# Kernel tuning notes

Hardware: AMD Instinct MI355X
Metric: run time of the kernel (lower is better)

The kernel has to match this reference:

```python
import jax, jax.numpy as jnp
import numpy as np

DEPTH = 8
DIM = 512
D_INNER = 2 * DIM          # mamba expand=2
D_STATE = 16
D_CONV = 4
DT_RANK = DIM // 16        # 32
B, H, W = 2, 16, 16
EPS = 1e-5


def setup_inputs() -> dict:
    key = jax.random.key(0)
    ks = jax.random.split(key, 8)
    s = 0.02
    f32 = jnp.float32
    x = jax.random.normal(ks[0], (B, DIM, H, W), f32)
    in_proj_w = (jax.random.normal(ks[1], (DEPTH, 2 * D_INNER, DIM), f32) * s)
    conv_w = (jax.random.normal(ks[2], (DEPTH, D_INNER, D_CONV), f32) * 0.1)
    conv_b = jnp.zeros((DEPTH, D_INNER), f32)
    x_proj_w = (jax.random.normal(ks[3], (DEPTH, DT_RANK + 2 * D_STATE, D_INNER), f32) * s)
    dt_proj_w = (jax.random.normal(ks[4], (DEPTH, D_INNER, DT_RANK), f32) * s)
    dt_proj_b = (jax.random.normal(ks[5], (DEPTH, D_INNER), f32) * 0.1)
    # S4D-real init: A = -exp(A_log), A_log = log(1..d_state)
    A_log = jnp.log(jnp.broadcast_to(
        jnp.arange(1, D_STATE + 1, dtype=f32), (DEPTH, D_INNER, D_STATE)))
    D = jnp.ones((DEPTH, D_INNER), f32)
    out_proj_w = (jax.random.normal(ks[6], (DEPTH, DIM, D_INNER), f32) * s)
    norm_w = jnp.ones((DEPTH, DIM), f32)
    final_norm_w = jnp.ones((DIM,), f32)
    return {"x": x, "in_proj_w": in_proj_w, "conv_w": conv_w, "conv_b": conv_b,
            "x_proj_w": x_proj_w, "dt_proj_w": dt_proj_w, "dt_proj_b": dt_proj_b,
            "A_log": A_log, "D": D, "out_proj_w": out_proj_w,
            "norm_w": norm_w, "final_norm_w": final_norm_w}


def _rmsnorm(x, w):
    # rms_norm_ref: no mean subtraction, weight only (bias is None)
    return x * jax.lax.rsqrt(jnp.mean(x * x, axis=-1, keepdims=True) + EPS) * w


def _mixer(h, Wi, cw, cb, Wx, Wdt, bdt, A_log, Dv, Wo):
    # h: [B, L, DIM]
    xz = jnp.einsum('bld,ed->ble', h, Wi)            # [B,L,2*Di]
    xc, z = jnp.split(xz, 2, axis=-1)
    # causal depthwise conv1d (pad left d_conv-1), then SiLU
    xt = xc.transpose(0, 2, 1)                        # [B,Di,L]
    xt = jax.lax.conv_general_dilated(
        xt, cw[:, None, :], (1,), [(D_CONV - 1, 0)],
        feature_group_count=D_INNER)
    xc = jax.nn.silu((xt + cb[None, :, None]).transpose(0, 2, 1))  # [B,L,Di]
    dbl = jnp.einsum('bld,kd->blk', xc, Wx)           # [B,L,dt_rank+2N]
    dtr = dbl[..., :DT_RANK]
    Bm = dbl[..., DT_RANK:DT_RANK + D_STATE]          # [B,L,N]
    Cm = dbl[..., DT_RANK + D_STATE:]                 # [B,L,N]
    dt = jax.nn.softplus(jnp.einsum('blr,dr->bld', dtr, Wdt) + bdt)  # [B,L,Di]
    A = -jnp.exp(A_log)                               # [Di,N]
    dA = jnp.exp(dt[..., None] * A)                   # [B,L,Di,N]
    dBx = (dt * xc)[..., None] * Bm[:, :, None, :]    # [B,L,Di,N]

    def step(s, inp):
        a, bx, c = inp
        s = a * s + bx                                # [B,Di,N]
        return s, jnp.einsum('bdn,bn->bd', s, c)

    s0 = jnp.zeros((xc.shape[0], D_INNER, D_STATE), xc.dtype)
    _, ys = jax.lax.scan(step, s0, (dA.transpose(1, 0, 2, 3),
                                    dBx.transpose(1, 0, 2, 3),
                                    Cm.transpose(1, 0, 2)))
    y = ys.transpose(1, 0, 2) + Dv * xc               # [B,L,Di]
    y = y * jax.nn.silu(z)
    return jnp.einsum('bld,od->blo', y, Wo)           # [B,L,DIM]


def reference(x, in_proj_w, conv_w, conv_b, x_proj_w, dt_proj_w, dt_proj_b,
              A_log, D, out_proj_w, norm_w, final_norm_w):
    Bz, C, Hh, Ww = x.shape
    h = x.reshape(Bz, C, Hh * Ww).transpose(0, 2, 1)  # [B,L,C]
    residual = None
    for i in range(DEPTH):
        # fused add + RMSNorm (prenorm): residual <- h + residual; hn = norm(residual)
        residual = h if residual is None else h + residual
        hn = _rmsnorm(residual, norm_w[i])
        h = _mixer(hn, in_proj_w[i], conv_w[i], conv_b[i], x_proj_w[i],
                   dt_proj_w[i], dt_proj_b[i], A_log[i], D[i], out_proj_w[i])
    # Original module: with return_index=[depth-1], the returned tensor is the
    # post-loop `residual`; the final mixer output and final norm are dead code.
    out = residual.reshape(Bz, Hh, Ww, C)
    return out.transpose(0, 3, 1, 2)
```

## Files before the change

kernel.cpp:

```cpp
#include <hip/hip_runtime.h>
#include <hip/hip_bf16.h>

typedef __bf16 bf16x8 __attribute__((ext_vector_type(8)));
typedef __bf16 bf16x4 __attribute__((ext_vector_type(4)));
typedef float  f32x4  __attribute__((ext_vector_type(4)));

#define DIM    512
#define DINNER 1024
#define SEQL   256
#define NLAYER 7
#define LPAD   260
#define NCH    8
#define CLEN   32

#define N4WI (NLAYER * 2048 * 512 / 4)
#define N4WX (NLAYER * 64 * 1024 / 4)
#define N4WO (NLAYER * 512 * 1024 / 4)
#define N4ALL (N4WI + N4WX + N4WO)
#define NCASTB (N4ALL / 256)

__global__ __launch_bounds__(256) void k_castin(const float* __restrict__ Wi,
                                                const float* __restrict__ Wx,
                                                const float* __restrict__ Wo,
                                                const float* __restrict__ x,
                                                __hip_bfloat16* __restrict__ wib,
                                                __hip_bfloat16* __restrict__ wxb,
                                                __hip_bfloat16* __restrict__ wob,
                                                float* __restrict__ res,
                                                float* __restrict__ dblraw) {
  if (blockIdx.x >= NCASTB + 1024) {
    int i = (blockIdx.x - NCASTB - 1024) * 256 + threadIdx.x;
    reinterpret_cast<float4*>(dblraw)[i] = float4{0.f, 0.f, 0.f, 0.f};
    return;
  }
  if (blockIdx.x >= NCASTB) {
    int idx = (blockIdx.x - NCASTB) * 256 + threadIdx.x;
    int d = idx & (DIM - 1), l = (idx >> 9) & (SEQL - 1), b = idx >> 17;
    res[idx] = x[((size_t)((b << 9) + d) << 8) + l];
    return;
  }
  int i = blockIdx.x * 256 + threadIdx.x;
  const float* src; __hip_bfloat16* dst; int j;
  if (i < N4WI)             { src = Wi; dst = wib; j = i; }
  else if (i < N4WI + N4WX) { src = Wx; dst = wxb; j = i - N4WI; }
  else                      { src = Wo; dst = wob; j = i - N4WI - N4WX; }
  float4 v = reinterpret_cast<const float4*>(src)[j];
  struct alignas(8) B4 { __hip_bfloat16 a, b, c, d; };
  B4 o{ (__hip_bfloat16)v.x, (__hip_bfloat16)v.y, (__hip_bfloat16)v.z, (__hip_bfloat16)v.w };
  reinterpret_cast<B4*>(dst)[j] = o;
}

__global__ __launch_bounds__(1024) void k_front(const float* __restrict__ res,
                                                const float* __restrict__ nwL,
                                                const __hip_bfloat16* __restrict__ wiL,
                                                const __hip_bfloat16* __restrict__ wxL,
                                                const float4* __restrict__ cwL,
                                                const float* __restrict__ cbL,
                                                __hip_bfloat16* __restrict__ xcb,
                                                float* __restrict__ zT,
                                                float* __restrict__ dblraw) {
  __shared__ __align__(16) char smem[79872];
  __hip_bfloat16 (*s_hn)[520] = (__hip_bfloat16(*)[520])smem;
  float (*s_xz)[132] = (float(*)[132])(smem + 49920);
  __hip_bfloat16 (*s_xcb)[72] = (__hip_bfloat16(*)[72])(smem + 75264);
  const int tid = threadIdx.x, bid = blockIdx.x;
  const int wid = tid >> 6, lane = tid & 63;
  const int r = lane & 15, g = lane >> 4;
  const int ttile = bid >> 4, sl = bid & 15;
  const int t0 = ttile * 32, m0 = t0 - 3;
#pragma unroll
  for (int k = 0; k < 3; ++k) {
    int rw = wid * 3 + k;
    int grc = min(max(m0 + rw, 0), 511);
    const float* rr = res + ((size_t)grc << 9);
    float v[8]; float ssum = 0.f;
#pragma unroll
    for (int j2 = 0; j2 < 8; ++j2) { v[j2] = rr[lane + (j2 << 6)]; ssum = fmaf(v[j2], v[j2], ssum); }
#pragma unroll
    for (int m = 1; m < 64; m <<= 1) ssum += __shfl_xor(ssum, m);
    float inv = rsqrtf(ssum * (1.0f / 512.0f) + 1e-5f);
#pragma unroll
    for (int j2 = 0; j2 < 8; ++j2)
      s_hn[rw][lane + (j2 << 6)] = (__hip_bfloat16)(v[j2] * inv * nwL[lane + (j2 << 6)]);
  }
  __syncthreads();
  for (int j = wid; j < 24; j += 16) {
    int mf = j >> 3, cf = j & 7;
    int gcol = (cf < 4) ? (sl * 64 + cf * 16 + r) : (1024 + sl * 64 + (cf - 4) * 16 + r);
    const bf16x8* pb = reinterpret_cast<const bf16x8*>(wiL + (size_t)gcol * 512) + g;
    f32x4 acc = {0.f, 0.f, 0.f, 0.f};
#pragma unroll
    for (int kc = 0; kc < 16; ++kc) {
      bf16x8 a = *reinterpret_cast<const bf16x8*>(&s_hn[mf * 16 + r][kc * 32 + g * 8]);
      acc = __builtin_amdgcn_mfma_f32_16x16x32_bf16(a, pb[kc * 4], acc, 0, 0, 0);
    }
    int cc = (cf < 4) ? (cf * 16 + r) : (64 + (cf - 4) * 16 + r);
#pragma unroll
    for (int jj = 0; jj < 4; ++jj) s_xz[mf * 16 + g * 4 + jj][cc] = acc[jj];
  }
  __syncthreads();
  const int t0s = t0 & 255;
#pragma unroll
  for (int k = 0; k < 2; ++k) {
    int e = tid + (k << 10);
    int lloc = e >> 6, c = e & 63;
    int gd = sl * 64 + c;
    int lseq = t0s + lloc;
    float4 wv = cwL[gd];
    float accv = cbL[gd];
    accv = fmaf(s_xz[lloc + 3][c], wv.w, accv);
    if (lseq >= 1) accv = fmaf(s_xz[lloc + 2][c], wv.z, accv);
    if (lseq >= 2) accv = fmaf(s_xz[lloc + 1][c], wv.y, accv);
    if (lseq >= 3) accv = fmaf(s_xz[lloc + 0][c], wv.x, accv);
    float sv = accv / (1.f + __expf(-accv));
    __hip_bfloat16 hb = (__hip_bfloat16)sv;
    xcb[(size_t)(t0 + lloc) * 1024 + gd] = hb;
    s_xcb[lloc][c] = hb;
  }
  __syncthreads();
  if (wid < 8) {
    int mf = wid & 1, nf = wid >> 1;
    f32x4 acc = {0.f, 0.f, 0.f, 0.f};
#pragma unroll
    for (int kc = 0; kc < 2; ++kc) {
      bf16x8 a = *reinterpret_cast<const bf16x8*>(&s_xcb[mf * 16 + r][kc * 32 + g * 8]);
      bf16x8 bb = *reinterpret_cast<const bf16x8*>(
          wxL + (size_t)(nf * 16 + r) * 1024 + sl * 64 + kc * 32 + g * 8);
      acc = __builtin_amdgcn_mfma_f32_16x16x32_bf16(a, bb, acc, 0, 0, 0);
    }
#pragma unroll
    for (int jj = 0; jj < 4; ++jj)
      atomicAdd(&dblraw[(size_t)(t0 + mf * 16 + g * 4 + jj) * 64 + nf * 16 + r], acc[jj]);
  } else {
#pragma unroll
    for (int k = 0; k < 4; ++k) {
      int e = (tid - 512) + (k << 9);
      int lloc = e & 31, c = e >> 5;
      int gd = sl * 64 + c;
      zT[(size_t)gd * 512 + t0 + lloc] = s_xz[lloc + 3][64 + c];
    }
  }
}

__global__ __launch_bounds__(512) void k_scan(const float* __restrict__ dblraw,
                                              const float* __restrict__ WdtL,
                                              const float* __restrict__ bdtL,
                                              const __hip_bfloat16* __restrict__ xcb,
                                              const float* __restrict__ zT,
                                              const float* __restrict__ alog,
                                              const float* __restrict__ dv,
                                              __hip_bfloat16* __restrict__ y) {
  __shared__ __align__(16) char smem[49792];
  float (*s_dt)[LPAD] = (float(*)[LPAD])(smem);
  float (*s_xc)[LPAD] = (float(*)[LPAD])(smem + 4160);
  float (*s_B)[LPAD]  = (float(*)[LPAD])(smem + 8320);
  float (*s_C)[LPAD]  = (float(*)[LPAD])(smem + 24960);
  float (*s_pe)[64]   = (float(*)[64]) (smem + 41600);
  float (*s_se)[64]   = (float(*)[64]) (smem + 43648);
  float (*s_ys)[4]    = (float(*)[4])  (smem + 45696);
  const int tid = threadIdx.x, bid = blockIdx.x;
  const int cg = tid >> 6;
  const int tt = tid & 63;
  const int n = tt & 15, dl = tt >> 4;
  const int b = bid >> 8;
  const int d0 = (bid & 255) << 2;
  const int d = d0 + dl;
  const int bL = b * SEQL;

#pragma unroll
  for (int k = 0; k < 4; ++k) {
    int fidx = tid + (k << 9);
    int l = fidx >> 3, q = fidx & 7;
    float4 v = *reinterpret_cast<const float4*>(dblraw + ((size_t)(bL + l) << 6) + 32 + (q << 2));
    float* dst = (q < 4) ? &s_B[(q & 3) << 2][l] : &s_C[(q & 3) << 2][l];
    dst[0] = v.x; dst[LPAD] = v.y; dst[2 * LPAD] = v.z; dst[3 * LPAD] = v.w;
  }
  if (tid < 256) {
    bf16x4 u = *reinterpret_cast<const bf16x4*>(xcb + (size_t)(bL + tid) * 1024 + d0);
#pragma unroll
    for (int e = 0; e < 4; ++e) s_xc[e][tid] = (float)u[e];
  }
  {
    int tk = tid >> 1;
    int cp = (tid & 1) << 1;
    const float* drow = dblraw + ((size_t)(bL + tk) << 6);
    float xv[32];
#pragma unroll
    for (int q = 0; q < 8; ++q) {
      float4 x4 = *reinterpret_cast<const float4*>(drow + (q << 2));
      xv[q * 4 + 0] = x4.x; xv[q * 4 + 1] = x4.y;
      xv[q * 4 + 2] = x4.z; xv[q * 4 + 3] = x4.w;
    }
#pragma unroll
    for (int kk = 0; kk < 2; ++kk) {
      int ch = cp + kk;
      const float4* wr = reinterpret_cast<const float4*>(WdtL + ((size_t)(d0 + ch) << 5));
      float acc = bdtL[d0 + ch];
#pragma unroll
      for (int q = 0; q < 8; ++q) {
        float4 w = wr[q];
        acc = fmaf(xv[q * 4 + 0], w.x, acc);
        acc = fmaf(xv[q * 4 + 1], w.y, acc);
        acc = fmaf(xv[q * 4 + 2], w.z, acc);
        acc = fmaf(xv[q * 4 + 3], w.w, acc);
      }
      s_dt[ch][tk] = (acc > 20.f) ? acc : log1pf(__expf(acc));
    }
  }
  __syncthreads();

  const float An = -__expf(alog[(size_t)d * 16 + n]);
  const int lb = cg << 5;

  float s = 0.f, P = 1.f;
#pragma unroll 2
  for (int l4 = 0; l4 < CLEN; l4 += 4) {
    const int l = lb + l4;
    float4 dt4 = *reinterpret_cast<const float4*>(&s_dt[dl][l]);
    float4 xc4 = *reinterpret_cast<const float4*>(&s_xc[dl][l]);
    float4 B4  = *reinterpret_cast<const float4*>(&s_B[n][l]);
    float dA;
    dA = __expf(dt4.x * An); P *= dA; s = fmaf(dA, s, dt4.x * xc4.x * B4.x);
    dA = __expf(dt4.y * An); P *= dA; s = fmaf(dA, s, dt4.y * xc4.y * B4.y);
    dA = __expf(dt4.z * An); P *= dA; s = fmaf(dA, s, dt4.z * xc4.z * B4.z);
    dA = __expf(dt4.w * An); P *= dA; s = fmaf(dA, s, dt4.w * xc4.w * B4.w);
  }
  s_pe[cg][tt] = P;
  s_se[cg][tt] = s;
  __syncthreads();

  float ss = 0.f;
  for (int c = 0; c < cg; ++c) ss = fmaf(s_pe[c][tt], ss, s_se[c][tt]);

  float s2 = ss;
#pragma unroll
  for (int half = 0; half < 2; ++half) {
    const int base = lb + (half << 4);
    float cr[16];
#pragma unroll
    for (int l4 = 0; l4 < 16; l4 += 4) {
      const int l = base + l4;
      float4 dt4 = *reinterpret_cast<const float4*>(&s_dt[dl][l]);
      float4 xc4 = *reinterpret_cast<const float4*>(&s_xc[dl][l]);
      float4 B4  = *reinterpret_cast<const float4*>(&s_B[n][l]);
      float4 C4  = *reinterpret_cast<const float4*>(&s_C[n][l]);
      float dA;
      dA = __expf(dt4.x * An); s2 = fmaf(dA, s2, dt4.x * xc4.x * B4.x); cr[l4 + 0] = s2 * C4.x;
      dA = __expf(dt4.y * An); s2 = fmaf(dA, s2, dt4.y * xc4.y * B4.y); cr[l4 + 1] = s2 * C4.y;
      dA = __expf(dt4.z * An); s2 = fmaf(dA, s2, dt4.z * xc4.z * B4.z); cr[l4 + 2] = s2 * C4.z;
      dA = __expf(dt4.w * An); s2 = fmaf(dA, s2, dt4.w * xc4.w * B4.w); cr[l4 + 3] = s2 * C4.w;
    }
#pragma unroll
    for (int i = 0; i < 16; ++i) {
      float c = cr[i];
      c += __shfl_xor(c, 1);
      c += __shfl_xor(c, 2);
      c += __shfl_xor(c, 4);
      c += __shfl_xor(c, 8);
      cr[i] = c;
    }
    if (n == 0) {
#pragma unroll
      for (int i = 0; i < 16; ++i) s_ys[base + i][dl] = cr[i];
    }
  }
  __syncthreads();

#pragma unroll
  for (int k = 0; k < 2; ++k) {
    int idx = tid + (k << 9);
    int l = idx >> 2, dd = idx & 3;
    float sum = s_ys[l][dd];
    float xcv = s_xc[dd][l];
    float zv = zT[(size_t)(d0 + dd) * 512 + bL + l];
    float yv = (sum + dv[d0 + dd] * xcv) * (zv / (1.f + __expf(-zv)));
    y[((size_t)(bL + l) << 10) + d0 + dd] = (__hip_bfloat16)yv;
  }
}

template <bool FINAL>
__global__ __launch_bounds__(1024) void k_outproj(const __hip_bfloat16* __restrict__ y,
                                                  const __hip_bfloat16* __restrict__ woL,
                                                  float* __restrict__ res,
                                                  float* __restrict__ out,
                                                  float* __restrict__ dblraw) {
  __shared__ __align__(16) float s_red[16 * 1088 + 32 * 33];
  float (*s_tr)[33] = (float(*)[33])(s_red + 16 * 1088);
  const int tid = threadIdx.x, bid = blockIdx.x;
  const int wid = tid >> 6, lane = tid & 63;
  const int r = lane & 15, g = lane >> 4;
  int tile = bid >> 2, q = bid & 3;
  int row0 = (tile >> 3) * 64 + ((q >> 1) << 5);
  int col0 = (tile & 7) * 64 + ((q & 1) << 5);
  if (!FINAL && tid < 32)
    reinterpret_cast<float4*>(dblraw)[bid * 32 + tid] = float4{0.f, 0.f, 0.f, 0.f};
  {
    const bf16x8* pa0 = reinterpret_cast<const bf16x8*>(y + (size_t)(row0 + r) * 1024) + g + wid * 8;
    const bf16x8* pa1 = reinterpret_cast<const bf16x8*>(y + (size_t)(row0 + 16 + r) * 1024) + g + wid * 8;
    const bf16x8* pb0 = reinterpret_cast<const bf16x8*>(woL + (size_t)(col0 + r) * 1024) + g + wid * 8;
    const bf16x8* pb1 = reinterpret_cast<const bf16x8*>(woL + (size_t)(col0 + 16 + r) * 1024) + g + wid * 8;
    f32x4 zz = {0.f, 0.f, 0.f, 0.f};
    f32x4 acc[4] = {zz, zz, zz, zz};
#pragma unroll
    for (int kc = 0; kc < 2; ++kc) {
      bf16x8 a0 = pa0[kc * 4], a1 = pa1[kc * 4];
      bf16x8 b0 = pb0[kc * 4], b1 = pb1[kc * 4];
      acc[0] = __builtin_amdgcn_mfma_f32_16x16x32_bf16(a0, b0, acc[0], 0, 0, 0);
      acc[1] = __builtin_amdgcn_mfma_f32_16x16x32_bf16(a0, b1, acc[1], 0, 0, 0);
      acc[2] = __builtin_amdgcn_mfma_f32_16x16x32_bf16(a1, b0, acc[2], 0, 0, 0);
      acc[3] = __builtin_amdgcn_mfma_f32_16x16x32_bf16(a1, b1, acc[3], 0, 0, 0);
    }
    float* sr = s_red + wid * 1088;
#pragma unroll
    for (int e = 0; e < 4; ++e)
#pragma unroll
      for (int jj = 0; jj < 4; ++jj)
        sr[(((e >> 1) << 4) + (g << 2) + jj) * 34 + ((e & 1) << 4) + r] = acc[e][jj];
  }
  __syncthreads();
  {
    int rrow = tid >> 5, rcol = tid & 31;
    float sum = 0.f;
#pragma unroll
    for (int w = 0; w < 16; ++w) sum += s_red[w * 1088 + rrow * 34 + rcol];
    if (!FINAL) {
      res[(size_t)(row0 + rrow) * 512 + col0 + rcol] += sum;
    } else {
      s_tr[rcol][rrow] = res[(size_t)(row0 + rrow) * 512 + col0 + rcol] + sum;
    }
  }
  if (FINAL) {
    __syncthreads();
    int tl = tid & 31, tc = tid >> 5;
    int b = row0 >> 8, l0 = row0 & 255;
    out[(((size_t)((b << 9) + col0 + tc)) << 8) | (l0 + tl)] = s_tr[tc][tl];
  }
}

extern "C" void kernel_launch(void* const* d_in, const int* in_sizes, int n_in,
                              void* d_out, int out_size, void* d_ws, size_t ws_size,
                              hipStream_t stream) {
  (void)in_sizes; (void)n_in; (void)out_size; (void)ws_size;
  const float* x    = (const float*)d_in[0];
  const float* Wi   = (const float*)d_in[1];
  const float* cw   = (const float*)d_in[2];
  const float* cb   = (const float*)d_in[3];
  const float* Wx   = (const float*)d_in[4];
  const float* Wdt  = (const float*)d_in[5];
  const float* bdt  = (const float*)d_in[6];
  const float* Alog = (const float*)d_in[7];
  const float* Dv   = (const float*)d_in[8];
  const float* Wo   = (const float*)d_in[9];
  const float* nw   = (const float*)d_in[10];

  char* ws = (char*)d_ws;
  float*          res    = (float*)(ws + 0);
  __hip_bfloat16* xcb    = (__hip_bfloat16*)(ws + 1048576);
  float*          zT     = (float*)(ws + 4194304);
  float*          dblraw = (float*)(ws + 6291456);
  __hip_bfloat16* y      = (__hip_bfloat16*)(ws + 8454144);
  __hip_bfloat16* wib    = (__hip_bfloat16*)(ws + 10485760);
  __hip_bfloat16* wxb    = (__hip_bfloat16*)(ws + 25165824);
  __hip_bfloat16* wob    = (__hip_bfloat16*)(ws + 26083328);

  k_castin<<<NCASTB + 1024 + 32, 256, 0, stream>>>(Wi, Wx, Wo, x, wib, wxb, wob,
                                                   res, dblraw);

  for (int L = 0; L < NLAYER; ++L) {
    k_front<<<256, 1024, 0, stream>>>(res, nw + L * DIM,
                                      wib + (size_t)L * 2048 * 512,
                                      wxb + (size_t)L * 64 * 1024,
                                      (const float4*)cw + (size_t)L * DINNER,
                                      cb + L * DINNER, xcb, zT, dblraw);
    k_scan<<<512, 512, 0, stream>>>(dblraw,
                                    Wdt + (size_t)L * DINNER * 32, bdt + L * DINNER,
                                    xcb, zT,
                                    Alog + (size_t)L * DINNER * 16, Dv + L * DINNER, y);
    if (L < NLAYER - 1)
      k_outproj<false><<<256, 1024, 0, stream>>>(y, wob + (size_t)L * 512 * 1024, res,
                                                 nullptr, dblraw);
    else
      k_outproj<true><<<256, 1024, 0, stream>>>(y, wob + (size_t)L * 512 * 1024, res,
                                                (float*)d_out, dblraw);
  }
}
```

Baseline: 302.5 us.

## Precompute RMSNorm sum-of-squares in outproj epilogue via atomics

Each row's sum of squares is now computed where the residual is written: the out-projection epilogue does a shuffle reduction and an atomicAdd into a per-row buffer, and the cast kernel seeds it for the first layer. The scan kernel zeroes this buffer between uses. The front kernel then skips its per-row reduction over 512 elements, which it previously repeated for overlapping halo rows in every block. In exchange the change adds float atomics, whose order is nondeterministic, and an extra dependency chain across three kernels.

```diff
diff --git a/kernel.cpp b/kernel.cpp
--- a/kernel.cpp
+++ b/kernel.cpp
@@ -27,7 +27,24 @@
                                                 __hip_bfloat16* __restrict__ wxb,
                                                 __hip_bfloat16* __restrict__ wob,
                                                 float* __restrict__ res,
-                                                float* __restrict__ dblraw) {
+                                                float* __restrict__ dblraw,
+                                                float* __restrict__ ssq) {
+  if (blockIdx.x >= NCASTB + 1024 + 32) {
+    int t = blockIdx.x - (NCASTB + 1024 + 32);
+    int b = t >> 8, l = t & 255;
+    const float* xb = x + ((size_t)b << 17) + l;
+    int tl = threadIdx.x;
+    float v0 = xb[(size_t)tl << 8];
+    float v1 = xb[(size_t)(tl + 256) << 8];
+    float p = v0 * v0 + v1 * v1;
+#pragma unroll
+    for (int m = 1; m < 64; m <<= 1) p += __shfl_xor(p, m);
+    __shared__ float sred[4];
+    if ((tl & 63) == 0) sred[tl >> 6] = p;
+    __syncthreads();
+    if (tl == 0) ssq[t] = (sred[0] + sred[1]) + (sred[2] + sred[3]);
+    return;
+  }
   if (blockIdx.x >= NCASTB + 1024) {
     int i = (blockIdx.x - NCASTB - 1024) * 256 + threadIdx.x;
     reinterpret_cast<float4*>(dblraw)[i] = float4{0.f, 0.f, 0.f, 0.f};
@@ -51,6 +68,7 @@
 }
 
 __global__ __launch_bounds__(1024) void k_front(const float* __restrict__ res,
+                                                const float* __restrict__ ssq,
                                                 const float* __restrict__ nwL,
                                                 const __hip_bfloat16* __restrict__ wiL,
                                                 const __hip_bfloat16* __restrict__ wxL,
@@ -73,15 +91,11 @@
     int rw = wid * 3 + k;
     int grc = min(max(m0 + rw, 0), 511);
     const float* rr = res + ((size_t)grc << 9);
-    float v[8]; float ssum = 0.f;
-#pragma unroll
-    for (int j2 = 0; j2 < 8; ++j2) { v[j2] = rr[lane + (j2 << 6)]; ssum = fmaf(v[j2], v[j2], ssum); }
-#pragma unroll
-    for (int m = 1; m < 64; m <<= 1) ssum += __shfl_xor(ssum, m);
-    float inv = rsqrtf(ssum * (1.0f / 512.0f) + 1e-5f);
+    float inv = rsqrtf(ssq[grc] * (1.0f / 512.0f) + 1e-5f);
 #pragma unroll
     for (int j2 = 0; j2 < 8; ++j2)
-      s_hn[rw][lane + (j2 << 6)] = (__hip_bfloat16)(v[j2] * inv * nwL[lane + (j2 << 6)]);
+      s_hn[rw][lane + (j2 << 6)] =
+          (__hip_bfloat16)(rr[lane + (j2 << 6)] * inv * nwL[lane + (j2 << 6)]);
   }
   __syncthreads();
   for (int j = wid; j < 24; j += 16) {
@@ -149,7 +163,8 @@
                                               const float* __restrict__ zT,
                                               const float* __restrict__ alog,
                                               const float* __restrict__ dv,
-                                              __hip_bfloat16* __restrict__ y) {
+                                              __hip_bfloat16* __restrict__ y,
+                                              float* __restrict__ ssqz) {
   __shared__ __align__(16) char smem[49792];
   float (*s_dt)[LPAD] = (float(*)[LPAD])(smem);
   float (*s_xc)[LPAD] = (float(*)[LPAD])(smem + 4160);
@@ -167,6 +182,8 @@
   const int d = d0 + dl;
   const int bL = b * SEQL;
 
+  if (bid < 2 && tid < 256) ssqz[(bid << 8) + tid] = 0.f;
+
 #pragma unroll
   for (int k = 0; k < 4; ++k) {
     int fidx = tid + (k << 9);
@@ -283,7 +300,8 @@
                                                   const __hip_bfloat16* __restrict__ woL,
                                                   float* __restrict__ res,
                                                   float* __restrict__ out,
-                                                  float* __restrict__ dblraw) {
+                                                  float* __restrict__ dblraw,
+                                                  float* __restrict__ ssq) {
   __shared__ __align__(16) float s_red[16 * 1088 + 32 * 33];
   float (*s_tr)[33] = (float(*)[33])(s_red + 16 * 1088);
   const int tid = threadIdx.x, bid = blockIdx.x;
@@ -324,7 +342,12 @@
 #pragma unroll
     for (int w = 0; w < 16; ++w) sum += s_red[w * 1088 + rrow * 34 + rcol];
     if (!FINAL) {
-      res[(size_t)(row0 + rrow) * 512 + col0 + rcol] += sum;
+      float val = res[(size_t)(row0 + rrow) * 512 + col0 + rcol] + sum;
+      res[(size_t)(row0 + rrow) * 512 + col0 + rcol] = val;
+      float p = val * val;
+      p += __shfl_xor(p, 1); p += __shfl_xor(p, 2); p += __shfl_xor(p, 4);
+      p += __shfl_xor(p, 8); p += __shfl_xor(p, 16);
+      if (rcol == 0) atomicAdd(&ssq[row0 + rrow], p);
     } else {
       s_tr[rcol][rrow] = res[(size_t)(row0 + rrow) * 512 + col0 + rcol] + sum;
     }
@@ -358,16 +381,18 @@
   __hip_bfloat16* xcb    = (__hip_bfloat16*)(ws + 1048576);
   float*          zT     = (float*)(ws + 4194304);
   float*          dblraw = (float*)(ws + 6291456);
+  float*          ssq    = (float*)(ws + 6422528);
   __hip_bfloat16* y      = (__hip_bfloat16*)(ws + 8454144);
   __hip_bfloat16* wib    = (__hip_bfloat16*)(ws + 10485760);
   __hip_bfloat16* wxb    = (__hip_bfloat16*)(ws + 25165824);
   __hip_bfloat16* wob    = (__hip_bfloat16*)(ws + 26083328);
 
-  k_castin<<<NCASTB + 1024 + 32, 256, 0, stream>>>(Wi, Wx, Wo, x, wib, wxb, wob,
-                                                   res, dblraw);
+  k_castin<<<NCASTB + 1024 + 32 + 512, 256, 0, stream>>>(Wi, Wx, Wo, x,
+                                                         wib, wxb, wob,
+                                                         res, dblraw, ssq);
 
   for (int L = 0; L < NLAYER; ++L) {
-    k_front<<<256, 1024, 0, stream>>>(res, nw + L * DIM,
+    k_front<<<256, 1024, 0, stream>>>(res, ssq, nw + L * DIM,
                                       wib + (size_t)L * 2048 * 512,
                                       wxb + (size_t)L * 64 * 1024,
                                       (const float4*)cw + (size_t)L * DINNER,
@@ -375,12 +400,13 @@
     k_scan<<<512, 512, 0, stream>>>(dblraw,
                                     Wdt + (size_t)L * DINNER * 32, bdt + L * DINNER,
                                     xcb, zT,
-                                    Alog + (size_t)L * DINNER * 16, Dv + L * DINNER, y);
+                                    Alog + (size_t)L * DINNER * 16, Dv + L * DINNER, y,
+                                    ssq);
     if (L < NLAYER - 1)
       k_outproj<false><<<256, 1024, 0, stream>>>(y, wob + (size_t)L * 512 * 1024, res,
-                                                 nullptr, dblraw);
+                                                 nullptr, dblraw, ssq);
     else
       k_outproj<true><<<256, 1024, 0, stream>>>(y, wob + (size_t)L * 512 * 1024, res,
-                                                (float*)d_out, dblraw);
+                                                (float*)d_out, dblraw, ssq);
   }
 }
```

Result: slower. 317.0 us (+4.8%).
